# Kernel optimization log

Hardware: AMD Instinct MI355X
Metric: run time of the kernel (lower is better)

## Reference

```python
import jax, jax.numpy as jnp
import numpy as np

ALPHA = 0.5  # config_param['alpha']


def setup_inputs() -> dict:
    key = jax.random.key(0)
    ks = jax.random.split(key, 10)
    B, T, N, E, H = 64, 20, 8192, 128, 128
    # sparse multi-hot basket indicators
    x = (jax.random.uniform(ks[0], (B, T, N)) < 0.01).astype(jnp.float32)
    seq_len = jax.random.randint(ks[1], (B,), 1, T + 1)  # pack_padded requires >=1
    A = jax.random.uniform(ks[2], (N, N), dtype=jnp.float32) * 0.01  # dense item-item adjacency
    W1 = jax.random.normal(ks[3], (E, N), dtype=jnp.float32) * 0.02
    b1 = jnp.zeros((E,), jnp.float32)
    W2 = jax.random.normal(ks[4], (E, N), dtype=jnp.float32) * 0.02
    b2 = jnp.zeros((E,), jnp.float32)
    W_ih = jax.random.normal(ks[5], (4 * H, E), dtype=jnp.float32) * 0.05
    W_hh = jax.random.normal(ks[6], (4 * H, H), dtype=jnp.float32) * 0.05
    b_ih = jnp.zeros((4 * H,), jnp.float32)
    b_hh = jnp.zeros((4 * H,), jnp.float32)
    W_out = jax.random.normal(ks[7], (N, H), dtype=jnp.float32) * 0.02
    I_B = jnp.ones((N,), jnp.float32) / N  # item_probs-style bias init
    threshold = jnp.array([0.005], jnp.float32)  # adj_matrix.mean()
    return dict(x=x, seq_len=seq_len, A=A, W1=W1, b1=b1, W2=W2, b2=b2,
                W_ih=W_ih, W_hh=W_hh, b_ih=b_ih, b_hh=b_hh,
                W_out=W_out, I_B=I_B, threshold=threshold)


def reference(x, seq_len, A, W1, b1, W2, b2, W_ih, W_hh, b_ih, b_hh, W_out, I_B, threshold):
    B, T, N = x.shape
    H = W_hh.shape[1]
    xf = x.reshape(B * T, N)
    # two basket encoders, elementwise max combine (dropout = identity in eval)
    e1 = jax.nn.relu(xf @ W1.T + b1)
    e2 = jax.nn.relu(xf @ W2.T + b2)
    basket = jnp.maximum(e1, e2).reshape(B, T, -1)  # [B, T, E]

    # 1-layer LSTM (torch gate order i,f,g,o); packed variable-length seqs
    # emulated by freezing (h, c) once t >= seq_len, so h_n matches pack_padded.
    valid = jnp.arange(T)[:, None] < seq_len[None, :]  # [T, B]
    xs = basket.transpose(1, 0, 2)                     # [T, B, E]
    b = b_ih + b_hh

    def step(carry, inp):
        h, c = carry
        x_t, v = inp
        gates = x_t @ W_ih.T + h @ W_hh.T + b
        i, f, g, o = jnp.split(gates, 4, axis=-1)
        c_new = jax.nn.sigmoid(f) * c + jax.nn.sigmoid(i) * jnp.tanh(g)
        h_new = jax.nn.sigmoid(o) * jnp.tanh(c_new)
        m = v[:, None]
        return (jnp.where(m, h_new, h), jnp.where(m, c_new, c)), None

    h0 = jnp.zeros((B, H), x.dtype)
    c0 = jnp.zeros((B, H), x.dtype)
    (h_n, _), _ = jax.lax.scan(step, (h0, c0), (xs, valid))

    p = jax.nn.sigmoid(h_n @ W_out.T)  # [B, N]
    # mm(p, diag(relu(I_B))) is algebraically an elementwise scale
    predict = (1.0 - ALPHA) * p + ALPHA * (p * jax.nn.relu(I_B) + jax.nn.relu(p @ A))
    return predict
```

## Files before the change

kernel.cpp:

```cpp
#include <hip/hip_runtime.h>
#include <hip/hip_bf16.h>
#include <stdint.h>

#define B_ 64
#define T_ 20
#define N_ 8192
#define E_ 128
#define H_ 128
#define G4 512
#define SPLITK 8

typedef short bf16x8 __attribute__((ext_vector_type(8)));
typedef float f32x4 __attribute__((ext_vector_type(4)));

__device__ __forceinline__ float sigmoidf_(float x){ return 1.0f/(1.0f+expf(-x)); }

__device__ __forceinline__ unsigned short f2bf(float f){
  union { float f; uint32_t u; } v; v.f = f;
  uint32_t u = v.u;
  uint32_t r = (u + 0x7FFFu + ((u >> 16) & 1u)) >> 16;
  return (unsigned short)r;
}
__device__ __forceinline__ uint32_t pk2(float a, float b){
  return (uint32_t)f2bf(a) | ((uint32_t)f2bf(b) << 16);
}
__device__ __forceinline__ float bf2f(unsigned short s){
  union { uint32_t u; float f; } v; v.u = ((uint32_t)s) << 16; return v.f;
}

__global__ void k_transpose(const float* __restrict__ W1, const float* __restrict__ W2,
                            float* __restrict__ W12T){
  __shared__ float t1[128][33];
  __shared__ float t2[128][33];
  int n0 = blockIdx.x * 32;
  int tid = threadIdx.x;
  int nl = tid & 31, eg = tid >> 5;
  for (int i = 0; i < 16; i++){
    int e = eg * 16 + i;
    t1[e][nl] = W1[(size_t)e*N_ + n0 + nl];
    t2[e][nl] = W2[(size_t)e*N_ + n0 + nl];
  }
  __syncthreads();
  for (int n = 0; n < 32; n++){
    float v = (tid < 128) ? t1[tid][n] : t2[tid-128][n];
    W12T[(size_t)(n0+n)*256 + tid] = v;
  }
}

__global__ void k_mlpx(const float* __restrict__ x, const int* __restrict__ seq_len,
                       const float* __restrict__ W12T, const float* __restrict__ b1,
                       const float* __restrict__ b2, const float* __restrict__ W_ih,
                       const float* __restrict__ b_ih, const float* __restrict__ b_hh,
                       float* __restrict__ Xp){
  int bt = blockIdx.x;
  int b = bt / T_, t = bt % T_;
  if (t >= seq_len[b]) return;
  __shared__ int idxs[1024];
  __shared__ int cnt;
  __shared__ float e2s[128];
  __shared__ float bx[128];
  int tid = threadIdx.x;
  if (tid == 0) cnt = 0;
  __syncthreads();
  const float4* xr = (const float4*)(x + (size_t)bt * N_);
  for (int i = 0; i < 8; i++){
    float4 v = xr[i*256 + tid];
    int base = (i*256 + tid)*4;
    if (v.x != 0.f){ int q = atomicAdd(&cnt,1); idxs[q] = base;   }
    if (v.y != 0.f){ int q = atomicAdd(&cnt,1); idxs[q] = base+1; }
    if (v.z != 0.f){ int q = atomicAdd(&cnt,1); idxs[q] = base+2; }
    if (v.w != 0.f){ int q = atomicAdd(&cnt,1); idxs[q] = base+3; }
  }
  __syncthreads();
  int m = cnt; if (m > 1024) m = 1024;
  float acc = (tid < 128) ? b1[tid] : b2[tid-128];
  int i = 0;
  for (; i + 8 <= m; i += 8){
    int j0 = idxs[i+0], j1 = idxs[i+1], j2 = idxs[i+2], j3 = idxs[i+3];
    int j4 = idxs[i+4], j5 = idxs[i+5], j6 = idxs[i+6], j7 = idxs[i+7];
    float v0 = W12T[(size_t)j0*256 + tid];
    float v1 = W12T[(size_t)j1*256 + tid];
    float v2 = W12T[(size_t)j2*256 + tid];
    float v3 = W12T[(size_t)j3*256 + tid];
    float v4 = W12T[(size_t)j4*256 + tid];
    float v5 = W12T[(size_t)j5*256 + tid];
    float v6 = W12T[(size_t)j6*256 + tid];
    float v7 = W12T[(size_t)j7*256 + tid];
    acc += ((v0+v1)+(v2+v3)) + ((v4+v5)+(v6+v7));
  }
  for (; i < m; i++)
    acc += W12T[(size_t)idxs[i]*256 + tid];
  acc = fmaxf(acc, 0.f);
  if (tid >= 128) e2s[tid-128] = acc;
  __syncthreads();
  if (tid < 128) bx[tid] = fmaxf(acc, e2s[tid]);
  __syncthreads();
  #pragma unroll
  for (int half = 0; half < 2; half++){
    int j = half*256 + tid;
    const float4* wr = (const float4*)(W_ih + (size_t)j * E_);
    float s0 = b_ih[j] + b_hh[j], s1 = 0.f, s2 = 0.f, s3 = 0.f;
    #pragma unroll
    for (int k4 = 0; k4 < 32; k4 += 4){
      float4 w, h;
      w = wr[k4+0]; h = *(const float4*)&bx[k4*4+ 0]; s0 += w.x*h.x + w.y*h.y + w.z*h.z + w.w*h.w;
      w = wr[k4+1]; h = *(const float4*)&bx[k4*4+ 4]; s1 += w.x*h.x + w.y*h.y + w.z*h.z + w.w*h.w;
      w = wr[k4+2]; h = *(const float4*)&bx[k4*4+ 8]; s2 += w.x*h.x + w.y*h.y + w.z*h.z + w.w*h.w;
      w = wr[k4+3]; h = *(const float4*)&bx[k4*4+12]; s3 += w.x*h.x + w.y*h.y + w.z*h.z + w.w*h.w;
    }
    Xp[(size_t)bt*G4 + j] = (s0 + s1) + (s2 + s3);
  }
}

__global__ void __launch_bounds__(512, 2)
k_lstm(const int* __restrict__ seq_len, const float* __restrict__ Xp,
       const float* __restrict__ W_hh, float* __restrict__ hn){
  int b = blockIdx.x;
  int L = seq_len[b];
  int j = threadIdx.x;
  float4 whh[32];
  const float4* wr = (const float4*)(W_hh + (size_t)j * H_);
  #pragma unroll
  for (int k = 0; k < 32; k++) whh[k] = wr[k];
  __shared__ float hs[128];
  __shared__ float gs[512];
  if (j < 128) hs[j] = 0.f;
  float c = 0.f;
  __syncthreads();
  for (int t = 0; t < L; t++){
    float s0 = Xp[((size_t)b*T_ + t)*G4 + j], s1 = 0.f, s2 = 0.f, s3 = 0.f;
    #pragma unroll
    for (int k = 0; k < 32; k += 4){
      float4 w, h;
      w = whh[k+0]; h = *(const float4*)&hs[k*4+ 0]; s0 += w.x*h.x + w.y*h.y + w.z*h.z + w.w*h.w;
      w = whh[k+1]; h = *(const float4*)&hs[k*4+ 4]; s1 += w.x*h.x + w.y*h.y + w.z*h.z + w.w*h.w;
      w = whh[k+2]; h = *(const float4*)&hs[k*4+ 8]; s2 += w.x*h.x + w.y*h.y + w.z*h.z + w.w*h.w;
      w = whh[k+3]; h = *(const float4*)&hs[k*4+12]; s3 += w.x*h.x + w.y*h.y + w.z*h.z + w.w*h.w;
    }
    gs[j] = (s0 + s1) + (s2 + s3);
    __syncthreads();
    if (j < 128){
      float i_ = gs[j], f_ = gs[128+j], gg = gs[256+j], o_ = gs[384+j];
      c = sigmoidf_(f_)*c + sigmoidf_(i_)*tanhf(gg);
      hs[j] = sigmoidf_(o_)*tanhf(c);
    }
    __syncthreads();
  }
  if (j < 128) hn[(size_t)b*H_ + j] = hs[j];
}

__global__ void k_pout(const float* __restrict__ hn, const float* __restrict__ W_out,
                       unsigned short* __restrict__ pbf){
  __shared__ unsigned short hb[64*128];
  int tid = threadIdx.x;
  {
    int row = tid >> 2;
    int k16 = (tid & 3) * 32;
    const float4* hr = (const float4*)(hn + (size_t)row*H_ + k16);
    #pragma unroll
    for (int i = 0; i < 4; i++){
      float4 a = hr[i*2], bq = hr[i*2+1];
      uint4 u; u.x = pk2(a.x,a.y); u.y = pk2(a.z,a.w); u.z = pk2(bq.x,bq.y); u.w = pk2(bq.z,bq.w);
      int blk = (k16 >> 3) + i;
      *(uint4*)&hb[row*128 + ((blk ^ (row & 7)) * 8)] = u;
    }
  }
  __syncthreads();
  int w = tid >> 6, l = tid & 63;
  int n0 = blockIdx.x * 128;
  f32x4 acc[8];
  #pragma unroll
  for (int i = 0; i < 8; i++) acc[i] = (f32x4){0.f,0.f,0.f,0.f};
  int row = w*16 + (l & 15);
  #pragma unroll
  for (int ks = 0; ks < 4; ks++){
    int kk = ks*32 + (l >> 4)*8;
    int blk = kk >> 3;
    bf16x8 af = *(bf16x8*)&hb[row*128 + ((blk ^ (row & 7)) * 8)];
    #pragma unroll
    for (int nt = 0; nt < 8; nt++){
      int n = n0 + nt*16 + (l & 15);
      const float4* wp = (const float4*)(W_out + (size_t)n*H_ + kk);
      float4 wa = wp[0], wb = wp[1];
      union { uint4 u; bf16x8 v; } cc;
      cc.u.x = pk2(wa.x,wa.y); cc.u.y = pk2(wa.z,wa.w);
      cc.u.z = pk2(wb.x,wb.y); cc.u.w = pk2(wb.z,wb.w);
      acc[nt] = __builtin_amdgcn_mfma_f32_16x16x32_bf16(af, cc.v, acc[nt], 0, 0, 0);
    }
  }
  #pragma unroll
  for (int nt = 0; nt < 8; nt++){
    int n = n0 + nt*16 + (l & 15);
    #pragma unroll
    for (int r = 0; r < 4; r++){
      int rr = w*16 + (l >> 4)*4 + r;
      float pv = 1.f/(1.f + expf(-acc[nt][r]));
      pbf[(size_t)rr*N_ + n] = f2bf(pv);
    }
  }
}

__global__ void __launch_bounds__(512, 4)
k_gemm(const unsigned short* __restrict__ pbf, const float* __restrict__ Ag,
       float* __restrict__ Cp){
  __shared__ unsigned short Abf0[128*64];
  __shared__ unsigned short Abf1[128*64];
  __shared__ unsigned short pt0[64*64];
  __shared__ unsigned short pt1[64*64];
  int tid = threadIdx.x;
  int nb = blockIdx.x & 63, ks = blockIdx.x >> 6;
  int n0 = nb * 128;
  int kbase = ks * (N_ / SPLITK);
  int sn = tid & 127, kq = tid >> 7;
  int prow = tid >> 3, c8 = tid & 7;
  int w = tid >> 6, l = tid & 63;
  int wm = w >> 2, wn = w & 3;
  f32x4 acc[2][2];
  #pragma unroll
  for (int i = 0; i < 2; i++)
    #pragma unroll
    for (int q = 0; q < 2; q++) acc[i][q] = (f32x4){0.f,0.f,0.f,0.f};
  float* Cout = Cp + (size_t)ks * (B_ * N_);
  const int NSTEP = (N_ / SPLITK) / 64;

  float aA[16], aB[16];
  uint4 pA, pB;

  auto issue = [&](float* ar, uint4& pr, int kb){
    pr = *(const uint4*)&pbf[(size_t)prow*N_ + kb + c8*8];
    #pragma unroll
    for (int i = 0; i < 4; i++){
      const float* base = Ag + (size_t)(kb + kq*16 + i*4)*N_ + n0 + sn;
      ar[i*4+0] = base[0];
      ar[i*4+1] = base[(size_t)N_];
      ar[i*4+2] = base[(size_t)2*N_];
      ar[i*4+3] = base[(size_t)3*N_];
    }
  };
  auto stage = [&](unsigned short* abf, unsigned short* ptb, const float* ar, const uint4& pr){
    *(uint4*)&ptb[prow*64 + ((c8*8) ^ ((prow & 7)*8))] = pr;
    #pragma unroll
    for (int i = 0; i < 4; i++){
      int k = kq*16 + i*4;
      uint2 u; u.x = pk2(ar[i*4+0], ar[i*4+1]); u.y = pk2(ar[i*4+2], ar[i*4+3]);
      *(uint2*)&abf[sn*64 + (k ^ ((sn & 7)*8))] = u;
    }
  };
  auto compute = [&](const unsigned short* abf, const unsigned short* ptb){
    #pragma unroll
    for (int kc = 0; kc < 64; kc += 32){
      int ko = kc + (l >> 4)*8;
      bf16x8 af[2], bfr[2];
      #pragma unroll
      for (int mi = 0; mi < 2; mi++){
        int r = wm*32 + mi*16 + (l & 15);
        af[mi] = *(const bf16x8*)&ptb[r*64 + (ko ^ ((r & 7)*8))];
      }
      #pragma unroll
      for (int ni = 0; ni < 2; ni++){
        int n = wn*32 + ni*16 + (l & 15);
        bfr[ni] = *(const bf16x8*)&abf[n*64 + (ko ^ ((n & 7)*8))];
      }
      #pragma unroll
      for (int mi = 0; mi < 2; mi++)
        #pragma unroll
        for (int ni = 0; ni < 2; ni++)
          acc[mi][ni] = __builtin_amdgcn_mfma_f32_16x16x32_bf16(af[mi], bfr[ni], acc[mi][ni], 0, 0, 0);
    }
  };

  issue(aA, pA, kbase);
  for (int s = 0; s < NSTEP; s += 2){
    if (s + 1 < NSTEP) issue(aB, pB, kbase + (s+1)*64);
    stage(Abf0, pt0, aA, pA);
    asm volatile("s_waitcnt lgkmcnt(0)" ::: "memory");
    __builtin_amdgcn_sched_barrier(0);
    __builtin_amdgcn_s_barrier();
    __builtin_amdgcn_sched_barrier(0);
    compute(Abf0, pt0);
    if (s + 2 < NSTEP) issue(aA, pA, kbase + (s+2)*64);
    stage(Abf1, pt1, aB, pB);
    asm volatile("s_waitcnt lgkmcnt(0)" ::: "memory");
    __builtin_amdgcn_sched_barrier(0);
    __builtin_amdgcn_s_barrier();
    __builtin_amdgcn_sched_barrier(0);
    compute(Abf1, pt1);
  }

  #pragma unroll
  for (int mi = 0; mi < 2; mi++)
    #pragma unroll
    for (int ni = 0; ni < 2; ni++){
      int n = n0 + wn*32 + ni*16 + (l & 15);
      #pragma unroll
      for (int r = 0; r < 4; r++){
        int rr = wm*32 + mi*16 + (l >> 4)*4 + r;
        Cout[(size_t)rr*N_ + n] = acc[mi][ni][r];
      }
    }
}

__global__ void k_final(const unsigned short* __restrict__ pbf, const float* __restrict__ Cp,
                        const float* __restrict__ I_B, float* __restrict__ out){
  int idx = blockIdx.x*256 + threadIdx.x;
  ushort4 pu = ((const ushort4*)pbf)[idx];
  float4 cv = {0.f, 0.f, 0.f, 0.f};
  #pragma unroll
  for (int s = 0; s < SPLITK; s++){
    float4 v = ((const float4*)(Cp + (size_t)s * (B_ * N_)))[idx];
    cv.x += v.x; cv.y += v.y; cv.z += v.z; cv.w += v.w;
  }
  int n = (idx*4) & (N_-1);
  float4 ib = *(const float4*)&I_B[n];
  float4 o;
  float p0 = bf2f(pu.x), p1 = bf2f(pu.y), p2 = bf2f(pu.z), p3 = bf2f(pu.w);
  o.x = 0.5f*p0 + 0.5f*(p0*fmaxf(ib.x,0.f) + fmaxf(cv.x,0.f));
  o.y = 0.5f*p1 + 0.5f*(p1*fmaxf(ib.y,0.f) + fmaxf(cv.y,0.f));
  o.z = 0.5f*p2 + 0.5f*(p2*fmaxf(ib.z,0.f) + fmaxf(cv.z,0.f));
  o.w = 0.5f*p3 + 0.5f*(p3*fmaxf(ib.w,0.f) + fmaxf(cv.w,0.f));
  ((float4*)out)[idx] = o;
}

extern "C" void kernel_launch(void* const* d_in, const int* in_sizes, int n_in,
                              void* d_out, int out_size, void* d_ws, size_t ws_size,
                              hipStream_t stream) {
  const float* x     = (const float*)d_in[0];
  const int*   seq   = (const int*)  d_in[1];
  const float* A     = (const float*)d_in[2];
  const float* W1    = (const float*)d_in[3];
  const float* b1    = (const float*)d_in[4];
  const float* W2    = (const float*)d_in[5];
  const float* b2    = (const float*)d_in[6];
  const float* W_ih  = (const float*)d_in[7];
  const float* W_hh  = (const float*)d_in[8];
  const float* b_ih  = (const float*)d_in[9];
  const float* b_hh  = (const float*)d_in[10];
  const float* W_out = (const float*)d_in[11];
  const float* I_B   = (const float*)d_in[12];
  float* out = (float*)d_out;

  float* ws   = (float*)d_ws;
  float* W12T = ws;
  float* Xp   = W12T + 2097152;
  float* hn   = Xp + 655360;
  float* Cp   = hn + 8192;
  unsigned short* pbf = (unsigned short*)(Cp + 4194304);

  k_transpose<<<256, 256, 0, stream>>>(W1, W2, W12T);
  k_mlpx     <<<1280,256, 0, stream>>>(x, seq, W12T, b1, b2, W_ih, b_ih, b_hh, Xp);
  k_lstm     <<<64,  512, 0, stream>>>(seq, Xp, W_hh, hn);
  k_pout     <<<64,  256, 0, stream>>>(hn, W_out, pbf);
  k_gemm     <<<64*SPLITK, 512, 0, stream>>>(pbf, A, Cp);
  k_final    <<<512, 256, 0, stream>>>(pbf, Cp, I_B, out);
}
```

Baseline: 177.7 us.

## Store encoder weights as bf16 and split input projection into MFMA GEMM

The transposed W1/W2 table is now stored in bf16, which halves the bytes gathered per nonzero in the sparse basket encoder. The per-row W_ih projection that k_mlpx did with scalar FMAs moves into a separate batched kernel using bf16 MFMA, with basket features staged through a swizzled LDS tile. This adds an extra kernel launch and an intermediate basket buffer, and introduces bf16 rounding in both the encoder and the input projection. Rows past seq_len now write zeros to the basket buffer.

After: 152.5 us. 14.2% less time.

```diff
diff --git a/kernel.cpp b/kernel.cpp
--- a/kernel.cpp
+++ b/kernel.cpp
@@ -29,7 +29,7 @@
 }
 
 __global__ void k_transpose(const float* __restrict__ W1, const float* __restrict__ W2,
-                            float* __restrict__ W12T){
+                            unsigned short* __restrict__ W12T){
   __shared__ float t1[128][33];
   __shared__ float t2[128][33];
   int n0 = blockIdx.x * 32;
@@ -43,23 +43,23 @@
   __syncthreads();
   for (int n = 0; n < 32; n++){
     float v = (tid < 128) ? t1[tid][n] : t2[tid-128][n];
-    W12T[(size_t)(n0+n)*256 + tid] = v;
-  }
-}
-
-__global__ void k_mlpx(const float* __restrict__ x, const int* __restrict__ seq_len,
-                       const float* __restrict__ W12T, const float* __restrict__ b1,
-                       const float* __restrict__ b2, const float* __restrict__ W_ih,
-                       const float* __restrict__ b_ih, const float* __restrict__ b_hh,
-                       float* __restrict__ Xp){
+    W12T[(size_t)(n0+n)*256 + tid] = f2bf(v);
+  }
+}
+
+__global__ void k_mlp(const float* __restrict__ x, const int* __restrict__ seq_len,
+                      const unsigned short* __restrict__ W12T, const float* __restrict__ b1,
+                      const float* __restrict__ b2, float* __restrict__ basket){
   int bt = blockIdx.x;
   int b = bt / T_, t = bt % T_;
-  if (t >= seq_len[b]) return;
+  int tid = threadIdx.x;
+  if (t >= seq_len[b]){
+    if (tid < 128) basket[(size_t)bt*E_ + tid] = 0.f;
+    return;
+  }
   __shared__ int idxs[1024];
   __shared__ int cnt;
   __shared__ float e2s[128];
-  __shared__ float bx[128];
-  int tid = threadIdx.x;
   if (tid == 0) cnt = 0;
   __syncthreads();
   const float4* xr = (const float4*)(x + (size_t)bt * N_);
@@ -78,37 +78,75 @@
   for (; i + 8 <= m; i += 8){
     int j0 = idxs[i+0], j1 = idxs[i+1], j2 = idxs[i+2], j3 = idxs[i+3];
     int j4 = idxs[i+4], j5 = idxs[i+5], j6 = idxs[i+6], j7 = idxs[i+7];
-    float v0 = W12T[(size_t)j0*256 + tid];
-    float v1 = W12T[(size_t)j1*256 + tid];
-    float v2 = W12T[(size_t)j2*256 + tid];
-    float v3 = W12T[(size_t)j3*256 + tid];
-    float v4 = W12T[(size_t)j4*256 + tid];
-    float v5 = W12T[(size_t)j5*256 + tid];
-    float v6 = W12T[(size_t)j6*256 + tid];
-    float v7 = W12T[(size_t)j7*256 + tid];
+    float v0 = bf2f(W12T[(size_t)j0*256 + tid]);
+    float v1 = bf2f(W12T[(size_t)j1*256 + tid]);
+    float v2 = bf2f(W12T[(size_t)j2*256 + tid]);
+    float v3 = bf2f(W12T[(size_t)j3*256 + tid]);
+    float v4 = bf2f(W12T[(size_t)j4*256 + tid]);
+    float v5 = bf2f(W12T[(size_t)j5*256 + tid]);
+    float v6 = bf2f(W12T[(size_t)j6*256 + tid]);
+    float v7 = bf2f(W12T[(size_t)j7*256 + tid]);
     acc += ((v0+v1)+(v2+v3)) + ((v4+v5)+(v6+v7));
   }
   for (; i < m; i++)
-    acc += W12T[(size_t)idxs[i]*256 + tid];
+    acc += bf2f(W12T[(size_t)idxs[i]*256 + tid]);
   acc = fmaxf(acc, 0.f);
   if (tid >= 128) e2s[tid-128] = acc;
   __syncthreads();
-  if (tid < 128) bx[tid] = fmaxf(acc, e2s[tid]);
-  __syncthreads();
-  #pragma unroll
-  for (int half = 0; half < 2; half++){
-    int j = half*256 + tid;
-    const float4* wr = (const float4*)(W_ih + (size_t)j * E_);
-    float s0 = b_ih[j] + b_hh[j], s1 = 0.f, s2 = 0.f, s3 = 0.f;
-    #pragma unroll
-    for (int k4 = 0; k4 < 32; k4 += 4){
-      float4 w, h;
-      w = wr[k4+0]; h = *(const float4*)&bx[k4*4+ 0]; s0 += w.x*h.x + w.y*h.y + w.z*h.z + w.w*h.w;
-      w = wr[k4+1]; h = *(const float4*)&bx[k4*4+ 4]; s1 += w.x*h.x + w.y*h.y + w.z*h.z + w.w*h.w;
-      w = wr[k4+2]; h = *(const float4*)&bx[k4*4+ 8]; s2 += w.x*h.x + w.y*h.y + w.z*h.z + w.w*h.w;
-      w = wr[k4+3]; h = *(const float4*)&bx[k4*4+12]; s3 += w.x*h.x + w.y*h.y + w.z*h.z + w.w*h.w;
-    }
-    Xp[(size_t)bt*G4 + j] = (s0 + s1) + (s2 + s3);
+  if (tid < 128) basket[(size_t)bt*E_ + tid] = fmaxf(acc, e2s[tid]);
+}
+
+__global__ void k_xgemm(const float* __restrict__ basket, const float* __restrict__ W_ih,
+                        const float* __restrict__ b_ih, const float* __restrict__ b_hh,
+                        float* __restrict__ Xp){
+  __shared__ unsigned short hb[64*128];
+  int tid = threadIdx.x;
+  int rt = blockIdx.x;
+  int ct = blockIdx.y;
+  {
+    int row = tid >> 2;
+    int k16 = (tid & 3) * 32;
+    const float4* hr = (const float4*)(basket + ((size_t)rt*64 + row)*E_ + k16);
+    #pragma unroll
+    for (int i = 0; i < 4; i++){
+      float4 a = hr[i*2], bq = hr[i*2+1];
+      uint4 u; u.x = pk2(a.x,a.y); u.y = pk2(a.z,a.w); u.z = pk2(bq.x,bq.y); u.w = pk2(bq.z,bq.w);
+      int blk = (k16 >> 3) + i;
+      *(uint4*)&hb[row*128 + ((blk ^ (row & 7)) * 8)] = u;
+    }
+  }
+  __syncthreads();
+  int w = tid >> 6, l = tid & 63;
+  int n0 = ct * 128;
+  f32x4 acc[8];
+  #pragma unroll
+  for (int i = 0; i < 8; i++) acc[i] = (f32x4){0.f,0.f,0.f,0.f};
+  int row = w*16 + (l & 15);
+  #pragma unroll
+  for (int ks = 0; ks < 4; ks++){
+    int kk = ks*32 + (l >> 4)*8;
+    int blk = kk >> 3;
+    bf16x8 af = *(bf16x8*)&hb[row*128 + ((blk ^ (row & 7)) * 8)];
+    #pragma unroll
+    for (int nt = 0; nt < 8; nt++){
+      int n = n0 + nt*16 + (l & 15);
+      const float4* wp = (const float4*)(W_ih + (size_t)n*E_ + kk);
+      float4 wa = wp[0], wb = wp[1];
+      union { uint4 u; bf16x8 v; } cc;
+      cc.u.x = pk2(wa.x,wa.y); cc.u.y = pk2(wa.z,wa.w);
+      cc.u.z = pk2(wb.x,wb.y); cc.u.w = pk2(wb.z,wb.w);
+      acc[nt] = __builtin_amdgcn_mfma_f32_16x16x32_bf16(af, cc.v, acc[nt], 0, 0, 0);
+    }
+  }
+  #pragma unroll
+  for (int nt = 0; nt < 8; nt++){
+    int n = n0 + nt*16 + (l & 15);
+    float bias = b_ih[n] + b_hh[n];
+    #pragma unroll
+    for (int r = 0; r < 4; r++){
+      int rr = w*16 + (l >> 4)*4 + r;
+      Xp[((size_t)rt*64 + rr)*G4 + n] = acc[nt][r] + bias;
+    }
   }
 }
 
@@ -340,14 +378,16 @@
   float* out = (float*)d_out;
 
   float* ws   = (float*)d_ws;
-  float* W12T = ws;
-  float* Xp   = W12T + 2097152;
-  float* hn   = Xp + 655360;
-  float* Cp   = hn + 8192;
+  unsigned short* W12T = (unsigned short*)ws;
+  float* basket = ws + 1048576;
+  float* Xp     = basket + 163840;
+  float* hn     = Xp + 655360;
+  float* Cp     = hn + 8192;
   unsigned short* pbf = (unsigned short*)(Cp + 4194304);
 
   k_transpose<<<256, 256, 0, stream>>>(W1, W2, W12T);
-  k_mlpx     <<<1280,256, 0, stream>>>(x, seq, W12T, b1, b2, W_ih, b_ih, b_hh, Xp);
+  k_mlp      <<<1280,256, 0, stream>>>(x, seq, W12T, b1, b2, basket);
+  k_xgemm    <<<dim3(20,4), 256, 0, stream>>>(basket, W_ih, b_ih, b_hh, Xp);
   k_lstm     <<<64,  512, 0, stream>>>(seq, Xp, W_hh, hn);
   k_pout     <<<64,  256, 0, stream>>>(hn, W_out, pbf);
   k_gemm     <<<64*SPLITK, 512, 0, stream>>>(pbf, A, Cp);
```
